# Optimization experiments

Hardware: AMD Instinct MI355X
Metric: run time of the kernel (lower is better)

The kernel has to match this reference:

```python
import jax, jax.numpy as jnp
import numpy as np

K = 5   # reassembly kernel size
G = 1   # group size
S = 2   # upsample scale factor


def setup_inputs() -> dict:
    key = jax.random.key(0)
    kf, km = jax.random.split(key)
    N, C, H, W = 4, 256, 64, 64
    features = jax.random.normal(kf, (N, C, H, W), dtype=jnp.float32)
    # masks: [N, K*K*G, H*S, W*S]; CARAFE masks are non-negative (softmax-normalized upstream)
    masks = jax.random.uniform(km, (N, K * K * G, H * S, W * S), dtype=jnp.float32)
    return {"features": features, "masks": masks}


def _carafe(features, masks, k=K, g=G, s=S):
    # features: [N, C, H, W]; masks: [N, k*k*g, H*s, W*s]
    N, C, H, W = features.shape
    pad = (k - 1) // 2
    fp = jnp.pad(features, ((0, 0), (0, 0), (pad, pad), (pad, pad)))
    # unfold k x k neighborhoods at LOW resolution: [N, C, k*k, H, W]
    patches = jnp.stack(
        [fp[:, :, i:i + H, j:j + W] for i in range(k) for j in range(k)], axis=2
    )
    cg = C // g
    patches = patches.reshape(N, g, cg, k * k, H, W)
    # mask channel layout is [group, k*k]; split output pixels (i = h*s + p)
    m = masks.reshape(N, g, k * k, H, s, W, s)
    # out[n,g,c,h,p,w,q] = sum_k m[n,g,k,h,p,w,q] * patches[n,g,c,k,h,w]
    out = jnp.einsum('ngkhpwq,ngckhw->ngchpwq', m, patches)
    return out.reshape(N, C, H * s, W * s)


def reference(features, masks):
    return _carafe(features, masks)
```

## Files before the change

kernel.cpp:

```cpp
#include <hip/hip_runtime.h>


#define CN 4
#define CC 256
#define CH 64
#define CW 64
#define CK 5
#define OH 128
#define OW 128

typedef float f32x2 __attribute__((ext_vector_type(2)));
typedef float f32x4 __attribute__((ext_vector_type(4)));

constexpr int TILE  = 16;
constexpr int SROWS = TILE + 4;
constexpr int LSTR  = 24;
constexpr int LBUF  = SROWS * LSTR;
constexpr int CPB   = 8;
constexpr int PPS   = CPB / 2;
constexpr int NTAP  = CK * CK;
constexpr int MQ    = 8;

__global__ __launch_bounds__(256, 4)
void carafe_kernel(const float* __restrict__ feat,
                   const float* __restrict__ masks,
                   float* __restrict__ out)
{
    __shared__ float2 lds[PPS * LBUF];

    const int tid  = threadIdx.x;
    const int wloc = tid & 15;
    const int hloc = tid >> 4;

    const int w0 = blockIdx.x * TILE;
    const int h0 = blockIdx.y * TILE;
    const int z  = blockIdx.z;
    const int n  = z >> 5;
    const int c0 = (z & 31) * CPB;

    const int oh0 = 2 * (h0 + hloc);
    const int ow0 = 2 * (w0 + wloc);
    const float* mp = masks + (((size_t)n * NTAP) * OH + oh0) * OW + ow0;

    float2 q0[MQ], q1[MQ];
#pragma unroll
    for (int t = 0; t < MQ; ++t) {
        q0[t] = *(const float2*)(mp + (size_t)t * (OH * OW));
        q1[t] = *(const float2*)(mp + (size_t)t * (OH * OW) + OW);
    }

    const int r  = tid / 10;
    const int qq = 2 * (tid % 10);
    const int gr = h0 - 2 + r;
    const int gc = w0 - 2 + qq;
    const bool sv = (tid < 200) & (gr >= 0) & (gr < CH) & (gc >= 0) & (gc <= CW - 2);
    const int goff = sv ? (gr * CW + gc) : 0;
    const int l    = r * LSTR + qq;

    const float* fbase = feat + (size_t)(n * CC + c0) * (CH * CW);

    float2 pa[PPS], pb[PPS];
#pragma unroll
    for (int p = 0; p < PPS; ++p) {
        const float* f0 = fbase + (size_t)(2 * p) * (CH * CW);
        pa[p] = sv ? *(const float2*)(f0 + goff) : make_float2(0.f, 0.f);
        pb[p] = sv ? *(const float2*)(f0 + CH * CW + goff) : make_float2(0.f, 0.f);
    }
    if (tid < 200) {
#pragma unroll
        for (int p = 0; p < PPS; ++p) {
            *(f32x4*)&lds[p * LBUF + l] = (f32x4){pa[p].x, pb[p].x, pa[p].y, pb[p].y};
        }
    }

    __syncthreads();

    float2 a0[CPB], a1[CPB];
#pragma unroll
    for (int c = 0; c < CPB; ++c) {
        a0[c] = make_float2(0.f, 0.f);
        a1[c] = make_float2(0.f, 0.f);
    }

    const float2* lb = &lds[hloc * LSTR + wloc];

#pragma unroll
    for (int t = 0; t < NTAP; ++t) {
        const int i = t / CK, j = t % CK;
        const int slot = t % MQ;
        const float2 cm0 = q0[slot];
        const float2 cm1 = q1[slot];

        if (t + MQ < NTAP) {
            q0[slot] = *(const float2*)(mp + (size_t)(t + MQ) * (OH * OW));
            q1[slot] = *(const float2*)(mp + (size_t)(t + MQ) * (OH * OW) + OW);
        }

        float2 f[PPS];
#pragma unroll
        for (int p = 0; p < PPS; ++p)
            f[p] = lb[p * LBUF + i * LSTR + j];

#pragma unroll
        for (int p = 0; p < PPS; ++p) {
            a0[2 * p].x     += cm0.x * f[p].x;  a0[2 * p].y     += cm0.y * f[p].x;
            a1[2 * p].x     += cm1.x * f[p].x;  a1[2 * p].y     += cm1.y * f[p].x;
            a0[2 * p + 1].x += cm0.x * f[p].y;  a0[2 * p + 1].y += cm0.y * f[p].y;
            a1[2 * p + 1].x += cm1.x * f[p].y;  a1[2 * p + 1].y += cm1.y * f[p].y;
        }
    }

    float* obase = out + (((size_t)(n * CC + c0) * OH + oh0) * OW + ow0);
#pragma unroll
    for (int c = 0; c < CPB; ++c) {
        float* op = obase + (size_t)c * (OH * OW);
        __builtin_nontemporal_store((f32x2){a0[c].x, a0[c].y}, (f32x2*)op);
        __builtin_nontemporal_store((f32x2){a1[c].x, a1[c].y}, (f32x2*)(op + OW));
    }
}

extern "C" void kernel_launch(void* const* d_in, const int* in_sizes, int n_in,
                              void* d_out, int out_size, void* d_ws, size_t ws_size,
                              hipStream_t stream) {
    const float* feat  = (const float*)d_in[0];
    const float* masks = (const float*)d_in[1];
    float* out = (float*)d_out;

    dim3 grid(CW / TILE, CH / TILE, CN * (CC / CPB));
    dim3 block(256);
    hipLaunchKernelGGL(carafe_kernel, grid, block, 0, stream, feat, masks, out);
}
```

Measured before the change: 102.0 us.

## Reuse register-resident masks across four channel phases with double-buffered LDS

```diff
diff --git a/kernel.cpp b/kernel.cpp
--- a/kernel.cpp
+++ b/kernel.cpp
@@ -16,17 +16,18 @@
 constexpr int SROWS = TILE + 4;
 constexpr int LSTR  = 24;
 constexpr int LBUF  = SROWS * LSTR;
-constexpr int CPB   = 8;
-constexpr int PPS   = CPB / 2;
+constexpr int GPC   = 8;
+constexpr int PPS   = GPC / 2;
+constexpr int NPH   = 4;
+constexpr int CPB   = GPC * NPH;
 constexpr int NTAP  = CK * CK;
-constexpr int MQ    = 8;
 
-__global__ __launch_bounds__(256, 4)
+__global__ __launch_bounds__(256, 2)
 void carafe_kernel(const float* __restrict__ feat,
                    const float* __restrict__ masks,
                    float* __restrict__ out)
 {
-    __shared__ float2 lds[PPS * LBUF];
+    __shared__ float2 lds[2 * PPS * LBUF];
 
     const int tid  = threadIdx.x;
     const int wloc = tid & 15;
@@ -35,18 +36,18 @@
     const int w0 = blockIdx.x * TILE;
     const int h0 = blockIdx.y * TILE;
     const int z  = blockIdx.z;
-    const int n  = z >> 5;
-    const int c0 = (z & 31) * CPB;
+    const int n  = z >> 3;
+    const int c0 = (z & 7) * CPB;
 
     const int oh0 = 2 * (h0 + hloc);
     const int ow0 = 2 * (w0 + wloc);
     const float* mp = masks + (((size_t)n * NTAP) * OH + oh0) * OW + ow0;
 
-    float2 q0[MQ], q1[MQ];
+    float2 m0[NTAP], m1[NTAP];
 #pragma unroll
-    for (int t = 0; t < MQ; ++t) {
-        q0[t] = *(const float2*)(mp + (size_t)t * (OH * OW));
-        q1[t] = *(const float2*)(mp + (size_t)t * (OH * OW) + OW);
+    for (int t = 0; t < NTAP; ++t) {
+        m0[t] = *(const float2*)(mp + (size_t)t * (OH * OW));
+        m1[t] = *(const float2*)(mp + (size_t)t * (OH * OW) + OW);
     }
 
     const int r  = tid / 10;
@@ -60,62 +61,73 @@
     const float* fbase = feat + (size_t)(n * CC + c0) * (CH * CW);
 
     float2 pa[PPS], pb[PPS];
-#pragma unroll
-    for (int p = 0; p < PPS; ++p) {
-        const float* f0 = fbase + (size_t)(2 * p) * (CH * CW);
-        pa[p] = sv ? *(const float2*)(f0 + goff) : make_float2(0.f, 0.f);
-        pb[p] = sv ? *(const float2*)(f0 + CH * CW + goff) : make_float2(0.f, 0.f);
-    }
-    if (tid < 200) {
+    auto loadPhase = [&](int ph) {
 #pragma unroll
         for (int p = 0; p < PPS; ++p) {
-            *(f32x4*)&lds[p * LBUF + l] = (f32x4){pa[p].x, pb[p].x, pa[p].y, pb[p].y};
+            const float* f0 = fbase + (size_t)(ph * GPC + 2 * p) * (CH * CW);
+            pa[p] = sv ? *(const float2*)(f0 + goff) : make_float2(0.f, 0.f);
+            pb[p] = sv ? *(const float2*)(f0 + CH * CW + goff) : make_float2(0.f, 0.f);
         }
-    }
+    };
+    auto writePhase = [&](int buf) {
+        if (tid < 200) {
+            float2* dst = &lds[buf * (PPS * LBUF)];
+#pragma unroll
+            for (int p = 0; p < PPS; ++p)
+                *(f32x4*)&dst[p * LBUF + l] = (f32x4){pa[p].x, pb[p].x, pa[p].y, pb[p].y};
+        }
+    };
 
-    __syncthreads();
-
-    float2 a0[CPB], a1[CPB];
-#pragma unroll
-    for (int c = 0; c < CPB; ++c) {
-        a0[c] = make_float2(0.f, 0.f);
-        a1[c] = make_float2(0.f, 0.f);
-    }
-
-    const float2* lb = &lds[hloc * LSTR + wloc];
+    loadPhase(0);
 
 #pragma unroll
-    for (int t = 0; t < NTAP; ++t) {
-        const int i = t / CK, j = t % CK;
-        const int slot = t % MQ;
-        const float2 cm0 = q0[slot];
-        const float2 cm1 = q1[slot];
+    for (int t = 0; t < NTAP; ++t)
+        asm volatile("" : "+v"(m0[t].x), "+v"(m0[t].y), "+v"(m1[t].x), "+v"(m1[t].y));
 
-        if (t + MQ < NTAP) {
-            q0[slot] = *(const float2*)(mp + (size_t)(t + MQ) * (OH * OW));
-            q1[slot] = *(const float2*)(mp + (size_t)(t + MQ) * (OH * OW) + OW);
+    writePhase(0);
+    loadPhase(1);
+
+    float* obase = out + (((size_t)(n * CC + c0) * OH + oh0) * OW + ow0);
+
+    for (int ph = 0; ph < NPH; ++ph) {
+        __syncthreads();
+
+        if (ph + 1 < NPH) writePhase((ph + 1) & 1);
+        if (ph + 2 < NPH) loadPhase(ph + 2);
+
+        const float2* lb = &lds[(ph & 1) * (PPS * LBUF) + hloc * LSTR + wloc];
+
+        float2 a0[GPC], a1[GPC];
+#pragma unroll
+        for (int c = 0; c < GPC; ++c) {
+            a0[c] = make_float2(0.f, 0.f);
+            a1[c] = make_float2(0.f, 0.f);
         }
 
-        float2 f[PPS];
 #pragma unroll
-        for (int p = 0; p < PPS; ++p)
-            f[p] = lb[p * LBUF + i * LSTR + j];
+        for (int t = 0; t < NTAP; ++t) {
+            const int i = t / CK, j = t % CK;
+            float2 f[PPS];
+#pragma unroll
+            for (int p = 0; p < PPS; ++p)
+                f[p] = lb[p * LBUF + i * LSTR + j];
 
 #pragma unroll
-        for (int p = 0; p < PPS; ++p) {
-            a0[2 * p].x     += cm0.x * f[p].x;  a0[2 * p].y     += cm0.y * f[p].x;
-            a1[2 * p].x     += cm1.x * f[p].x;  a1[2 * p].y     += cm1.y * f[p].x;
-            a0[2 * p + 1].x += cm0.x * f[p].y;  a0[2 * p + 1].y += cm0.y * f[p].y;
-            a1[2 * p + 1].x += cm1.x * f[p].y;  a1[2 * p + 1].y += cm1.y * f[p].y;
+            for (int p = 0; p < PPS; ++p) {
+                a0[2 * p].x     += m0[t].x * f[p].x;  a0[2 * p].y     += m0[t].y * f[p].x;
+                a1[2 * p].x     += m1[t].x * f[p].x;  a1[2 * p].y     += m1[t].y * f[p].x;
+                a0[2 * p + 1].x += m0[t].x * f[p].y;  a0[2 * p + 1].y += m0[t].y * f[p].y;
+                a1[2 * p + 1].x += m1[t].x * f[p].y;  a1[2 * p + 1].y += m1[t].y * f[p].y;
+            }
         }
-    }
 
-    float* obase = out + (((size_t)(n * CC + c0) * OH + oh0) * OW + ow0);
+        float* opb = obase + (size_t)(ph * GPC) * (OH * OW);
 #pragma unroll
-    for (int c = 0; c < CPB; ++c) {
-        float* op = obase + (size_t)c * (OH * OW);
-        __builtin_nontemporal_store((f32x2){a0[c].x, a0[c].y}, (f32x2*)op);
-        __builtin_nontemporal_store((f32x2){a1[c].x, a1[c].y}, (f32x2*)(op + OW));
+        for (int c = 0; c < GPC; ++c) {
+            float* op = opb + (size_t)c * (OH * OW);
+            *(f32x2*)op        = (f32x2){a0[c].x, a0[c].y};
+            *(f32x2*)(op + OW) = (f32x2){a1[c].x, a1[c].y};
+        }
     }
 }
 
```

Result: faster. 99.73 us (-2.3%).
